# Optimization experiments

Measured on AMD Instinct MI355X. Metric: run time of the kernel, lower is better.

Reference implementation:

```python
import jax, jax.numpy as jnp
import numpy as np

B, R, T = 128, 36, 40
E, V, H1, H2, PH, VOC = 1024, 2048, 1024, 1024, 256, 10000


def _lstm_cell(x, h, c, Wi, Wh, b):
    # torch gate order: i, f, g, o
    g = x @ Wi.T + h @ Wh.T + b
    i, f, gg, o = jnp.split(g, 4, axis=-1)
    c_new = jax.nn.sigmoid(f) * c + jax.nn.sigmoid(i) * jnp.tanh(gg)
    h_new = jax.nn.sigmoid(o) * jnp.tanh(c_new)
    return h_new, c_new


def setup_inputs() -> dict:
    key = jax.random.key(0)
    ks = jax.random.split(key, 20)
    s = 0.05
    Vmat = jax.random.normal(ks[0], (B, R, V), jnp.float32)
    enc_features = jax.random.normal(ks[1], (B, V), jnp.float32)
    union_vfeats = jax.random.normal(ks[2], (B, V), jnp.float32)
    captions = jax.random.randint(ks[3], (B, T), 0, VOC, jnp.int32)
    lengths = jax.random.randint(ks[4], (B,), 1, T + 1, jnp.int32)
    lengths = jnp.sort(lengths)[::-1].at[0].set(T)  # sorted descending, max first
    embed_W = jax.random.normal(ks[5], (VOC, E), jnp.float32) * s
    Wi1 = jax.random.normal(ks[6], (4 * H1, H2 + V + E), jnp.float32) * s
    Wh1 = jax.random.normal(ks[7], (4 * H1, H1), jnp.float32) * s
    b1 = jax.random.normal(ks[8], (4 * H1,), jnp.float32) * s
    Wi2 = jax.random.normal(ks[9], (4 * H2, H1 + V), jnp.float32) * s
    Wh2 = jax.random.normal(ks[10], (4 * H2, H2), jnp.float32) * s
    b2 = jax.random.normal(ks[11], (4 * H2,), jnp.float32) * s
    Wva = jax.random.normal(ks[12], (PH, V), jnp.float32) * s
    bva = jax.random.normal(ks[13], (PH,), jnp.float32) * s
    Wha = jax.random.normal(ks[14], (PH, H1), jnp.float32) * s
    bha = jax.random.normal(ks[15], (PH,), jnp.float32) * s
    wa = jax.random.normal(ks[16], (PH,), jnp.float32) * s
    ba = jax.random.normal(ks[17], (), jnp.float32) * s
    Wl = jax.random.normal(ks[18], (VOC, H2), jnp.float32) * s
    bl = jax.random.normal(ks[19], (VOC,), jnp.float32) * s
    return dict(Vmat=Vmat, enc_features=enc_features, union_vfeats=union_vfeats,
                captions=captions, lengths=lengths, embed_W=embed_W,
                Wi1=Wi1, Wh1=Wh1, b1=b1, Wi2=Wi2, Wh2=Wh2, b2=b2,
                Wva=Wva, bva=bva, Wha=Wha, bha=bha, wa=wa, ba=ba, Wl=Wl, bl=bl)


def reference(Vmat, enc_features, union_vfeats, captions, lengths, embed_W,
              Wi1, Wh1, b1, Wi2, Wh2, b2, Wva, bva, Wha, bha, wa, ba, Wl, bl):
    embeddings = embed_W[captions]                      # [B, T, E]
    Va = Vmat @ Wva.T + bva                             # [B, R, PH] (precompute, step-invariant)

    def step(carry, xs):
        h1, c1, h2, c2 = carry
        emb_t, i = xs
        active = (lengths > i)[:, None]                 # [B, 1]
        x1 = jnp.concatenate([h2, union_vfeats, emb_t], axis=-1)
        h1n, c1n = _lstm_cell(x1, h1, c1, Wi1, Wh1, b1)
        # top-down attention over R regions
        logit = jnp.tanh(Va + (h1n @ Wha.T + bha)[:, None, :]) @ wa + ba  # [B, R]
        atten = jax.nn.softmax(logit, axis=1)
        av = jnp.einsum('br,brd->bd', atten, Vmat)      # [B, V]
        x2 = jnp.concatenate([av, h1n], axis=-1)
        h2n, c2n = _lstm_cell(x2, h2, c2, Wi2, Wh2, b2)
        logits = h2n @ Wl.T + bl                        # [B, VOC]
        # state freeze + zero outputs for finished sequences (ragged masking)
        h1 = jnp.where(active, h1n, h1); c1 = jnp.where(active, c1n, c1)
        h2 = jnp.where(active, h2n, h2); c2 = jnp.where(active, c2n, c2)
        out_t = jnp.where(active, logits, 0.0)
        return (h1, c1, h2, c2), out_t

    z1 = jnp.zeros((B, H1), jnp.float32)
    z2 = jnp.zeros((B, H2), jnp.float32)
    xs = (jnp.transpose(embeddings, (1, 0, 2)), jnp.arange(T, dtype=jnp.int32))
    _, outs = jax.lax.scan(step, (z1, z1, z2, z2), xs)  # [T, B, VOC]
    return jnp.transpose(outs, (1, 0, 2))               # [B, T, VOC]
```

## Files before the change

kernel.cpp:

```cpp
#include <hip/hip_runtime.h>

#define EPI_PART 0
#define EPI_BF16D 1

#define T_ 40
#define VOC_ 10000

typedef __attribute__((ext_vector_type(8))) short bf16x8;
typedef __attribute__((ext_vector_type(4))) short short4v;
typedef __attribute__((ext_vector_type(8))) short short8v;
typedef __attribute__((ext_vector_type(4))) float float4v;
typedef __attribute__((ext_vector_type(4))) float f32x4;

__device__ __forceinline__ float bf2f(short s) {
  unsigned u = ((unsigned)(unsigned short)s) << 16;
  float f; __builtin_memcpy(&f, &u, 4); return f;
}
__device__ __forceinline__ short f2bf(float f) {
  unsigned u; __builtin_memcpy(&u, &f, 4);
  u += 0x7FFFu + ((u >> 16) & 1u);
  return (short)(u >> 16);
}
__device__ __forceinline__ float sigm(float x) { return 1.f / (1.f + expf(-x)); }

__device__ __forceinline__ size_t pkidx(int row, int k, int K) {
  return (size_t)(row >> 4) * 16 * K + (size_t)(k >> 3) * 128 + (size_t)((row & 15) * 8 + (k & 7));
}


__global__ __launch_bounds__(256) void k_f2bf_split(const float* __restrict__ s,
    short* __restrict__ dh, short* __restrict__ dl, long n4) {
  long i = (long)blockIdx.x * 256 + threadIdx.x;
  long stride = (long)gridDim.x * 256;
  for (; i < n4; i += stride) {
    float4v f = ((const float4v*)s)[i];
    short4v oh, ol;
    #pragma unroll
    for (int j = 0; j < 4; j++) {
      short h = f2bf(f[j]); oh[j] = h; ol[j] = f2bf(f[j] - bf2f(h));
    }
    ((short4v*)dh)[i] = oh;
    ((short4v*)dl)[i] = ol;
  }
}

__global__ __launch_bounds__(256) void k_permpk(short* __restrict__ dh, short* __restrict__ dl,
    const float* __restrict__ s1, int ld1, int col0, int K1,
    const float* __restrict__ s2, int ld2, int Ktot) {
  int K4 = Ktot >> 2;
  long n4 = 4096L * K4;
  long stride = (long)gridDim.x * 256;
  for (long i = (long)blockIdx.x * 256 + threadIdx.x; i < n4; i += stride) {
    int p = (int)(i / K4);
    int c = ((int)(i % K4)) << 2;
    int orig = ((p & 3) << 10) + (p >> 2);
    const float* src = (c < K1) ? (s1 + (long)orig * ld1 + col0 + c)
                                : (s2 + (long)orig * ld2 + (c - K1));
    float4v f = *(const float4v*)src;
    short4v oh, ol;
    #pragma unroll
    for (int j = 0; j < 4; j++) {
      short h = f2bf(f[j]); oh[j] = h; ol[j] = f2bf(f[j] - bf2f(h));
    }
    size_t d = pkidx(p, c, Ktot);
    *(short4v*)&dh[d] = oh;
    if (dl) *(short4v*)&dl[d] = ol;
  }
}

__global__ __launch_bounds__(256) void k_packpk(short* __restrict__ dh, short* __restrict__ dl,
    const float* __restrict__ src, int ld, int Nr, int Nsrc, int K) {
  int K4 = K >> 2;
  long n4 = (long)Nr * K4;
  long stride = (long)gridDim.x * 256;
  for (long i = (long)blockIdx.x * 256 + threadIdx.x; i < n4; i += stride) {
    int row = (int)(i / K4);
    int c = ((int)(i % K4)) << 2;
    float4v f = {0.f, 0.f, 0.f, 0.f};
    if (row < Nsrc) f = *(const float4v*)(src + (long)row * ld + c);
    short4v oh, ol;
    #pragma unroll
    for (int j = 0; j < 4; j++) {
      short h = f2bf(f[j]); oh[j] = h; ol[j] = f2bf(f[j] - bf2f(h));
    }
    size_t d = pkidx(row, c, K);
    *(short4v*)&dh[d] = oh;
    if (dl) *(short4v*)&dl[d] = ol;
  }
}

__global__ __launch_bounds__(256) void k_perm_bias(float* __restrict__ d1, const float* __restrict__ s1,
                                                   float* __restrict__ d2, const float* __restrict__ s2) {
  int p = blockIdx.x * 256 + threadIdx.x;
  if (p < 4096) {
    int orig = ((p & 3) << 10) + (p >> 2);
    d1[p] = s1[orig];
    d2[p] = s2[orig];
  }
}

__global__ __launch_bounds__(256) void k_gather_emb(short* __restrict__ dst, const float* __restrict__ embW,
                                                    const int* __restrict__ cap) {
  int i = blockIdx.x * 256 + threadIdx.x;
  if (i >= 5120 * 128) return;
  int row = i >> 7, c8 = (i & 127) << 3;
  int tok = cap[row];
  const float4v* s = (const float4v*)(embW + (long)tok * 1024 + c8);
  float4v f0 = s[0], f1 = s[1];
  short8v o;
  #pragma unroll
  for (int j = 0; j < 4; j++) { o[j] = f2bf(f0[j]); o[4 + j] = f2bf(f1[j]); }
  *(short8v*)(dst + (long)row * 1024 + c8) = o;
}

__global__ __launch_bounds__(256) void k_pack_whaf(float* __restrict__ dst, const float* __restrict__ Wha) {
  int i = blockIdx.x * 256 + threadIdx.x;
  int hb = i >> 8, ph = i & 255;
  float4v a = *(const float4v*)(Wha + (long)ph * 1024 + hb * 8);
  float4v b4 = *(const float4v*)(Wha + (long)ph * 1024 + hb * 8 + 4);
  *(float4v*)(dst + ((long)hb * 256 + ph) * 8) = a;
  *(float4v*)(dst + ((long)hb * 256 + ph) * 8 + 4) = b4;
}


template<int NCS, bool SA, bool SW, int EPI>
__global__ __launch_bounds__(256) void k_g5(
    const short* __restrict__ A, const short* __restrict__ Alo, int lda,
    const short* __restrict__ W, const short* __restrict__ Wlo, int K,
    int Npad, int Mtot,
    float* __restrict__ outf, short* __restrict__ outbf) {
  __shared__ short sh[SA ? 16384 : 8192];
  const int tid = threadIdx.x;
  const int l = tid & 63, w = tid >> 6;
  const int rif = l & 15, kg = l >> 4;
  const int n0 = blockIdx.x * 64;
  const int k0 = blockIdx.y * NCS * 64;
  const int mbase = blockIdx.z * 128;

  f32x4 acc[8];
  #pragma unroll
  for (int m = 0; m < 8; m++) acc[m] = (f32x4){0.f, 0.f, 0.f, 0.f};

  bf16x8 wh[2][2], wl[2][2];
  const size_t wtile = (size_t)(n0 / 16 + w) * 16 * K + (size_t)l * 8;
  auto loadW = [&](int c, int slot) {
    size_t base = wtile + (size_t)((k0 + c * 64) >> 3) * 128;
    #pragma unroll
    for (int sk = 0; sk < 2; sk++) {
      wh[slot][sk] = *(const bf16x8*)(W + base + sk * 512);
      if (SW) wl[slot][sk] = *(const bf16x8*)(Wlo + base + sk * 512);
    }
  };

  short8v rA[4], rL[4];
  const int srow = tid >> 3;
  const int scol = (tid & 7) * 8;
  auto ldA = [&](int c) {
    #pragma unroll
    for (int j = 0; j < 4; j++) {
      size_t g = (size_t)(mbase + j * 32 + srow) * lda + k0 + c * 64 + scol;
      rA[j] = *(const short8v*)(A + g);
      if (SA) rL[j] = *(const short8v*)(Alo + g);
    }
  };
  auto stA = [&]() {
    #pragma unroll
    for (int j = 0; j < 4; j++) {
      int row = j * 32 + srow;
      int idx = row * 64 + (scol ^ ((row & 7) << 3));
      *(short8v*)&sh[idx] = rA[j];
      if (SA) *(short8v*)&sh[8192 + idx] = rL[j];
    }
  };
  auto compute = [&](int slot) {
    #pragma unroll
    for (int sk = 0; sk < 2; sk++) {
      int colb = ((sk * 32 + kg * 8) ^ ((rif & 7) << 3));
      #pragma unroll
      for (int m = 0; m < 8; m++) {
        int idx = (m * 16 + rif) * 64 + colb;
        bf16x8 ah = *(const bf16x8*)&sh[idx];
        acc[m] = __builtin_amdgcn_mfma_f32_16x16x32_bf16(ah, wh[slot][sk], acc[m], 0, 0, 0);
        if (SA) {
          bf16x8 al = *(const bf16x8*)&sh[8192 + idx];
          acc[m] = __builtin_amdgcn_mfma_f32_16x16x32_bf16(al, wh[slot][sk], acc[m], 0, 0, 0);
        }
        if (SW) acc[m] = __builtin_amdgcn_mfma_f32_16x16x32_bf16(ah, wl[slot][sk], acc[m], 0, 0, 0);
      }
    }
  };

  ldA(0); loadW(0, 0);
  stA();
  __syncthreads();
  #pragma unroll
  for (int c = 0; c < NCS; c++) {
    if (c + 1 < NCS) { ldA(c + 1); loadW(c + 1, (c + 1) & 1); }
    compute(c & 1);
    __syncthreads();
    if (c + 1 < NCS) { stA(); __syncthreads(); }
  }

  const int colw = n0 + w * 16 + rif;
  #pragma unroll
  for (int m = 0; m < 8; m++) {
    #pragma unroll
    for (int j = 0; j < 4; j++) {
      int row = m * 16 + kg * 4 + j;
      if constexpr (EPI == EPI_PART) {
        outf[((size_t)blockIdx.y * Mtot + mbase + row) * Npad + colw] = acc[m][j];
      } else {
        outbf[(size_t)(mbase + row) * Npad + colw] = f2bf(acc[m][j]);
      }
    }
  }
}

__global__ __launch_bounds__(256) void k_sum(const float* __restrict__ part,
    float* __restrict__ out, const float* __restrict__ bias,
    long n4, int N4, int KS, long stride4) {
  long i = (long)blockIdx.x * 256 + threadIdx.x;
  if (i >= n4) return;
  float4v a = *(const float4v*)&bias[(i % N4) * 4];
  for (int s = 0; s < KS; s++) {
    float4v p = ((const float4v*)part)[s * stride4 + i];
    #pragma unroll
    for (int j = 0; j < 4; j++) a[j] += p[j];
  }
  ((float4v*)out)[i] = a;
}

__global__ __launch_bounds__(256) void k_epi2(
    const float* __restrict__ part, const float* __restrict__ b2p,
    float* __restrict__ cstate,
    const short* __restrict__ xcur_hi, const short* __restrict__ xcur_lo,
    short* __restrict__ xnext_hi, short* __restrict__ xnext_lo,
    short* __restrict__ h2n_hi, short* __restrict__ h2n_lo,
    const int* __restrict__ lengths, int t) {
  int i = blockIdx.x * 256 + threadIdx.x;
  int b = i >> 10, h = i & 1023;
  float4v g = *(const float4v*)&b2p[h * 4];
  #pragma unroll
  for (int s = 0; s < 8; s++) {
    float4v p = *(const float4v*)&part[((size_t)s * 128 + b) * 4096 + h * 4];
    #pragma unroll
    for (int j = 0; j < 4; j++) g[j] += p[j];
  }
  float co = cstate[b * 1024 + h];
  float cn = sigm(g[1]) * co + sigm(g[0]) * tanhf(g[2]);
  float hn = sigm(g[3]) * tanhf(cn);
  bool act = lengths[b] > t;
  cstate[b * 1024 + h] = act ? cn : co;
  short hi16 = f2bf(hn);
  short lo16 = f2bf(hn - bf2f(hi16));
  h2n_hi[b * 1024 + h] = hi16;
  h2n_lo[b * 1024 + h] = lo16;
  short oh = xcur_hi[b * 2048 + h];
  short ol = xcur_lo[b * 2048 + h];
  xnext_hi[b * 2048 + h] = act ? hi16 : oh;
  xnext_lo[b * 2048 + h] = act ? lo16 : ol;
}

__global__ __launch_bounds__(256) void k_epi_logits(const float* __restrict__ part,
    const float* __restrict__ bl, const int* __restrict__ lengths, int t,
    float* __restrict__ out) {
  int id = blockIdx.x * 256 + threadIdx.x;
  if (id >= 320000) return;
  int b = id / 2500, q = (id % 2500) * 4;
  bool act = lengths[b] > t;
  float4v a = {0.f, 0.f, 0.f, 0.f};
  if (act) {
    a = *(const float4v*)&bl[q];
    #pragma unroll
    for (int s = 0; s < 4; s++) {
      float4v p = *(const float4v*)&part[((size_t)s * 128 + b) * 10048 + q];
      #pragma unroll
      for (int j = 0; j < 4; j++) a[j] += p[j];
    }
  }
  *(float4v*)&out[((size_t)b * T_ + t) * VOC_ + q] = a;
}

__global__ __launch_bounds__(256) void k_attn2(
    const float* __restrict__ partG,
    const float* __restrict__ zuv, const short* __restrict__ zemb,
    float* __restrict__ c1,
    const short* __restrict__ xcH, const short* __restrict__ xcL,
    short* __restrict__ xnH, short* __restrict__ xnL,
    short* __restrict__ x2H, short* __restrict__ x2L,
    const float* __restrict__ WhaF,
    const float* __restrict__ bha, const float* __restrict__ wa,
    const float* __restrict__ ba, const float* __restrict__ Va,
    const float* __restrict__ Vmat,
    const int* __restrict__ lengths, int t) {
  const int b = blockIdx.x, tid = threadIdx.x;
  __shared__ float h1f[1024];
  __shared__ float ha_sh[256];
  __shared__ float wa_sh[256];
  __shared__ float logit_sh[40];
  __shared__ float p_sh[40];
  const bool act = lengths[b] > t;
  #pragma unroll
  for (int i = 0; i < 4; i++) {
    int h = i * 256 + tid;
    float4v g = {0.f, 0.f, 0.f, 0.f};
    #pragma unroll
    for (int s = 0; s < 8; s++) {
      float4v p = *(const float4v*)&partG[((size_t)s * 128 + b) * 4096 + h * 4];
      #pragma unroll
      for (int j = 0; j < 4; j++) g[j] += p[j];
    }
    float4v z = *(const float4v*)&zuv[(size_t)b * 4096 + h * 4];
    short4v e4 = *(const short4v*)&zemb[((size_t)b * T_ + t) * 4096 + h * 4];
    #pragma unroll
    for (int j = 0; j < 4; j++) g[j] += z[j] + bf2f(e4[j]);
    float co = c1[b * 1024 + h];
    float cn = sigm(g[1]) * co + sigm(g[0]) * tanhf(g[2]);
    float hn = sigm(g[3]) * tanhf(cn);
    c1[b * 1024 + h] = act ? cn : co;
    h1f[h] = hn;
    short hi16 = f2bf(hn);
    short lo16 = f2bf(hn - bf2f(hi16));
    x2H[b * 4096 + 2048 + h] = hi16;
    x2L[b * 4096 + 2048 + h] = lo16;
    short oh = xcH[b * 2048 + 1024 + h];
    short ol = xcL[b * 2048 + 1024 + h];
    xnH[b * 2048 + 1024 + h] = act ? hi16 : oh;
    xnL[b * 2048 + 1024 + h] = act ? lo16 : ol;
    x2H[b * 4096 + 3072 + h] = xcH[b * 2048 + h];
    x2L[b * 4096 + 3072 + h] = xcL[b * 2048 + h];
  }
  wa_sh[tid] = wa[tid];
  __syncthreads();
  {
    float a = 0.f;
    const float* wp = WhaF + tid * 8;
    #pragma unroll 4
    for (int hb = 0; hb < 128; hb++) {
      float4v w0 = *(const float4v*)(wp + (size_t)hb * 2048);
      float4v w1 = *(const float4v*)(wp + (size_t)hb * 2048 + 4);
      #pragma unroll
      for (int j = 0; j < 4; j++) a += w0[j] * h1f[hb * 8 + j] + w1[j] * h1f[hb * 8 + 4 + j];
    }
    ha_sh[tid] = a + bha[tid];
  }
  __syncthreads();
  {
    const int r0 = tid >> 3, sl = tid & 7;
    const float ba0 = ba[0];
    for (int r = r0; r < 36; r += 32) {
      const float4v* va4 = (const float4v*)(Va + ((long)b * 36 + r) * 256 + sl * 32);
      float part = 0.f;
      #pragma unroll
      for (int q = 0; q < 8; q++) {
        float4v v4 = va4[q];
        #pragma unroll
        for (int j = 0; j < 4; j++) {
          int ph = sl * 32 + q * 4 + j;
          part += tanhf(v4[j] + ha_sh[ph]) * wa_sh[ph];
        }
      }
      part += __shfl_down(part, 4, 8);
      part += __shfl_down(part, 2, 8);
      part += __shfl_down(part, 1, 8);
      if (sl == 0) logit_sh[r] = part + ba0;
    }
  }
  __syncthreads();
  if (tid < 64) {
    float v = (tid < 36) ? logit_sh[tid] : -3.4e38f;
    float m = v;
    #pragma unroll
    for (int off = 32; off > 0; off >>= 1) m = fmaxf(m, __shfl_xor(m, off));
    float e = (tid < 36) ? expf(v - m) : 0.f;
    float s = e;
    #pragma unroll
    for (int off = 32; off > 0; off >>= 1) s += __shfl_xor(s, off);
    if (tid < 36) p_sh[tid] = e / s;
  }
  __syncthreads();
  {
    float av[8];
    #pragma unroll
    for (int j = 0; j < 8; j++) av[j] = 0.f;
    const float* vb = Vmat + (long)b * (36 * 2048) + tid * 8;
    for (int r = 0; r < 36; r++) {
      float p = p_sh[r];
      float4v v0 = *(const float4v*)(vb + (long)r * 2048);
      float4v v1 = *(const float4v*)(vb + (long)r * 2048 + 4);
      #pragma unroll
      for (int j = 0; j < 4; j++) { av[j] += p * v0[j]; av[4 + j] += p * v1[j]; }
    }
    short8v oh, ol;
    #pragma unroll
    for (int j = 0; j < 8; j++) {
      short h = f2bf(av[j]);
      oh[j] = h;
      ol[j] = f2bf(av[j] - bf2f(h));
    }
    *(short8v*)(x2H + b * 4096 + tid * 8) = oh;
    *(short8v*)(x2L + b * 4096 + tid * 8) = ol;
  }
}

extern "C" void kernel_launch(void* const* d_in, const int* in_sizes, int n_in,
                              void* d_out, int out_size, void* d_ws, size_t ws_size,
                              hipStream_t stream) {
  const float* Vmat = (const float*)d_in[0];
  const float* uv   = (const float*)d_in[2];
  const int* captions = (const int*)d_in[3];
  const int* lengths  = (const int*)d_in[4];
  const float* embW = (const float*)d_in[5];
  const float* Wi1 = (const float*)d_in[6];
  const float* Wh1 = (const float*)d_in[7];
  const float* b1  = (const float*)d_in[8];
  const float* Wi2 = (const float*)d_in[9];
  const float* Wh2 = (const float*)d_in[10];
  const float* b2  = (const float*)d_in[11];
  const float* Wva = (const float*)d_in[12];
  const float* bva = (const float*)d_in[13];
  const float* Wha = (const float*)d_in[14];
  const float* bha = (const float*)d_in[15];
  const float* wa  = (const float*)d_in[16];
  const float* ba  = (const float*)d_in[17];
  const float* Wl  = (const float*)d_in[18];
  const float* bl  = (const float*)d_in[19];
  (void)in_sizes; (void)n_in; (void)out_size; (void)ws_size;

  char* ws = (char*)d_ws;
  size_t off = 0;
  auto alloc = [&](size_t bytes) { void* p = ws + off; off += (bytes + 255) & ~255UL; return p; };
  short* W1dHi = (short*)alloc(4096L * 2048 * 2);
  short* W1dLo = (short*)alloc(4096L * 2048 * 2);
  short* W2dHi = (short*)alloc(4096L * 4096 * 2);
  short* W2dLo = (short*)alloc(4096L * 4096 * 2);
  short* WlPK  = (short*)alloc(10048L * 1024 * 2);
  float* WhaF  = (float*)alloc(128L * 256 * 8 * 4);
  float* VaBuf = (float*)alloc(4608L * 256 * 4);
  float* Z1uvB = (float*)alloc(128L * 4096 * 4);
  short* Z1embB = (short*)alloc(5120L * 4096 * 2);
  float* partG = (float*)alloc(4L * 128 * 10048 * 4);
  float* b1P = (float*)alloc(4096 * 4);
  float* b2P = (float*)alloc(4096 * 4);
  short* x1Hi = (short*)alloc(2L * 128 * 2048 * 2);
  short* x1Lo = (short*)alloc(2L * 128 * 2048 * 2);
  short* x2Hi = (short*)alloc(128L * 4096 * 2);
  short* x2Lo = (short*)alloc(128L * 4096 * 2);
  short* h2nHi = (short*)alloc(128L * 1024 * 2);
  short* h2nLo = (short*)alloc(128L * 1024 * 2);
  float* c1 = (float*)alloc(128L * 1024 * 4);
  float* c2 = (float*)alloc(128L * 1024 * 4);

  short* W1uvHi = W2dHi;
  short* W1uvLo = W2dHi + 4096L * 2048;
  float* zuvPart = (float*)(W2dHi + 4096L * 4096);
  short* uvHi = W2dHi + 4096L * 4096 + 4096L * 2048 + 2097152;
  short* uvLo = uvHi + 128L * 2048;
  short* WvaHi = uvLo + 128L * 2048;
  short* WvaLo = WvaHi + 256L * 2048;
  float* vaPart = (float*)W2dHi;
  short* W1ePk = (short*)partG;
  short* AembBF = (short*)partG + 4096L * 1024;
  short* VmatHi = Z1embB;
  short* VmatLo = Z1embB + 4608L * 2048;

  (void)hipMemsetAsync(x1Hi, 0, 2L * 128 * 2048 * 2, stream);
  (void)hipMemsetAsync(x1Lo, 0, 2L * 128 * 2048 * 2, stream);
  (void)hipMemsetAsync(c1, 0, 128L * 1024 * 4, stream);
  (void)hipMemsetAsync(c2, 0, 128L * 1024 * 4, stream);

  k_packpk<<<2048, 256, 0, stream>>>(WlPK, nullptr, Wl, 1024, 10048, 10000, 1024);
  k_pack_whaf<<<128, 256, 0, stream>>>(WhaF, Wha);
  k_packpk<<<512, 256, 0, stream>>>(WvaHi, WvaLo, Wva, 2048, 256, 256, 2048);
  k_permpk<<<2048, 256, 0, stream>>>(W1dHi, W1dLo, Wi1, 4096, 0, 1024, Wh1, 1024, 2048);
  k_permpk<<<2048, 256, 0, stream>>>(W1uvHi, W1uvLo, Wi1, 4096, 1024, 2048, Wi1, 4096, 2048);
  k_permpk<<<1024, 256, 0, stream>>>(W1ePk, nullptr, Wi1, 4096, 3072, 1024, Wi1, 4096, 1024);
  k_perm_bias<<<16, 256, 0, stream>>>(b1P, b1, b2P, b2);
  k_gather_emb<<<2560, 256, 0, stream>>>(AembBF, embW, captions);
  k_f2bf_split<<<2048, 256, 0, stream>>>(Vmat, VmatHi, VmatLo, 128L * 36 * 2048 / 4);
  k_f2bf_split<<<64, 256, 0, stream>>>(uv, uvHi, uvLo, 128L * 2048 / 4);

  k_g5<4, true, true, EPI_PART><<<dim3(64, 8, 1), 256, 0, stream>>>(
      uvHi, uvLo, 2048, W1uvHi, W1uvLo, 2048, 4096, 128, zuvPart, nullptr);
  k_sum<<<512, 256, 0, stream>>>(zuvPart, Z1uvB, b1P, 131072, 1024, 8, 131072);
  k_g5<4, true, true, EPI_PART><<<dim3(4, 8, 36), 256, 0, stream>>>(
      VmatHi, VmatLo, 2048, WvaHi, WvaLo, 2048, 256, 4608, vaPart, nullptr);
  k_sum<<<1152, 256, 0, stream>>>(vaPart, VaBuf, bva, 294912, 64, 8, 294912);
  k_permpk<<<4096, 256, 0, stream>>>(W2dHi, W2dLo, Wi2, 3072, 0, 3072, Wh2, 1024, 4096);
  k_g5<16, false, false, EPI_BF16D><<<dim3(64, 1, 40), 256, 0, stream>>>(
      AembBF, nullptr, 1024, W1ePk, nullptr, 1024, 4096, 5120, nullptr, Z1embB);

  for (int t = 0; t < T_; t++) {
    const short* xcH = x1Hi + (size_t)(t & 1) * (128 * 2048);
    const short* xcL = x1Lo + (size_t)(t & 1) * (128 * 2048);
    short* xnH = x1Hi + (size_t)((t + 1) & 1) * (128 * 2048);
    short* xnL = x1Lo + (size_t)((t + 1) & 1) * (128 * 2048);
    k_g5<4, true, true, EPI_PART><<<dim3(64, 8, 1), 256, 0, stream>>>(
        xcH, xcL, 2048, W1dHi, W1dLo, 2048, 4096, 128, partG, nullptr);
    k_attn2<<<128, 256, 0, stream>>>(partG, Z1uvB, Z1embB, c1,
        xcH, xcL, xnH, xnL, x2Hi, x2Lo, WhaF, bha, wa, ba, VaBuf, Vmat, lengths, t);
    k_g5<8, true, true, EPI_PART><<<dim3(64, 8, 1), 256, 0, stream>>>(
        x2Hi, x2Lo, 4096, W2dHi, W2dLo, 4096, 4096, 128, partG, nullptr);
    k_epi2<<<512, 256, 0, stream>>>(partG, b2P, c2,
        xcH, xcL, xnH, xnL, h2nHi, h2nLo, lengths, t);
    k_g5<4, true, false, EPI_PART><<<dim3(157, 4, 1), 256, 0, stream>>>(
        h2nHi, h2nLo, 1024, WlPK, nullptr, 1024, 10048, 128, partG, nullptr);
    k_epi_logits<<<1250, 256, 0, stream>>>(partG, bl, lengths, t, (float*)d_out);
  }
}
```

Baseline: 4.154 ms.

## Widen GEMM tiles and overlap vocab projection with next step's LSTM1 GEMM

The GEMM kernel now computes 128-wide N tiles, two 16-column fragments per wave, so each A tile loaded into shared memory is reused across twice as many outputs. The timestep loop is software-pipelined. The output-vocab GEMM for step t-1 runs in the same launch as the LSTM1 gate GEMM for step t, and its epilogue runs alongside the attention kernel, cutting launches and filling the GPU with more concurrent blocks. This needs an extra loop iteration, a padded Wl packing to 10112 columns and separate partial buffers. It also doubles the weight registers per thread, which may lower occupancy.

```diff
diff --git a/kernel.cpp b/kernel.cpp
--- a/kernel.cpp
+++ b/kernel.cpp
@@ -124,31 +124,37 @@
 
 
 template<int NCS, bool SA, bool SW, int EPI>
-__global__ __launch_bounds__(256) void k_g5(
+__device__ __forceinline__ void gemm_body(short* sh, int bx, int ks, int mb,
     const short* __restrict__ A, const short* __restrict__ Alo, int lda,
     const short* __restrict__ W, const short* __restrict__ Wlo, int K,
-    int Npad, int Mtot,
-    float* __restrict__ outf, short* __restrict__ outbf) {
-  __shared__ short sh[SA ? 16384 : 8192];
+    int Npad, int Mtot, float* __restrict__ part, short* __restrict__ outbf) {
   const int tid = threadIdx.x;
   const int l = tid & 63, w = tid >> 6;
   const int rif = l & 15, kg = l >> 4;
-  const int n0 = blockIdx.x * 64;
-  const int k0 = blockIdx.y * NCS * 64;
-  const int mbase = blockIdx.z * 128;
-
-  f32x4 acc[8];
+  const int n0 = bx * 128;
+  const int k0 = ks * NCS * 64;
+  const int mbase = mb * 128;
+
+  f32x4 acc[8][2];
   #pragma unroll
-  for (int m = 0; m < 8; m++) acc[m] = (f32x4){0.f, 0.f, 0.f, 0.f};
-
-  bf16x8 wh[2][2], wl[2][2];
-  const size_t wtile = (size_t)(n0 / 16 + w) * 16 * K + (size_t)l * 8;
+  for (int m = 0; m < 8; m++) {
+    acc[m][0] = (f32x4){0.f, 0.f, 0.f, 0.f};
+    acc[m][1] = (f32x4){0.f, 0.f, 0.f, 0.f};
+  }
+
+  bf16x8 wh[2][2][2], wl[2][2][2];
+  size_t wt0 = (size_t)(n0 / 16 + w * 2) * 16 * K + (size_t)l * 8;
+  size_t wt1 = wt0 + (size_t)16 * K;
   auto loadW = [&](int c, int slot) {
-    size_t base = wtile + (size_t)((k0 + c * 64) >> 3) * 128;
+    size_t base = (size_t)((k0 + c * 64) >> 3) * 128;
     #pragma unroll
     for (int sk = 0; sk < 2; sk++) {
-      wh[slot][sk] = *(const bf16x8*)(W + base + sk * 512);
-      if (SW) wl[slot][sk] = *(const bf16x8*)(Wlo + base + sk * 512);
+      wh[slot][sk][0] = *(const bf16x8*)(W + wt0 + base + sk * 512);
+      wh[slot][sk][1] = *(const bf16x8*)(W + wt1 + base + sk * 512);
+      if (SW) {
+        wl[slot][sk][0] = *(const bf16x8*)(Wlo + wt0 + base + sk * 512);
+        wl[slot][sk][1] = *(const bf16x8*)(Wlo + wt1 + base + sk * 512);
+      }
     }
   };
 
@@ -180,12 +186,14 @@
       for (int m = 0; m < 8; m++) {
         int idx = (m * 16 + rif) * 64 + colb;
         bf16x8 ah = *(const bf16x8*)&sh[idx];
-        acc[m] = __builtin_amdgcn_mfma_f32_16x16x32_bf16(ah, wh[slot][sk], acc[m], 0, 0, 0);
-        if (SA) {
-          bf16x8 al = *(const bf16x8*)&sh[8192 + idx];
-          acc[m] = __builtin_amdgcn_mfma_f32_16x16x32_bf16(al, wh[slot][sk], acc[m], 0, 0, 0);
+        bf16x8 al;
+        if (SA) al = *(const bf16x8*)&sh[8192 + idx];
+        #pragma unroll
+        for (int nf = 0; nf < 2; nf++) {
+          acc[m][nf] = __builtin_amdgcn_mfma_f32_16x16x32_bf16(ah, wh[slot][0][nf] * 0 + wh[slot][sk][nf], acc[m][nf], 0, 0, 0);
+          if (SA) acc[m][nf] = __builtin_amdgcn_mfma_f32_16x16x32_bf16(al, wh[slot][sk][nf], acc[m][nf], 0, 0, 0);
+          if (SW) acc[m][nf] = __builtin_amdgcn_mfma_f32_16x16x32_bf16(ah, wl[slot][sk][nf], acc[m][nf], 0, 0, 0);
         }
-        if (SW) acc[m] = __builtin_amdgcn_mfma_f32_16x16x32_bf16(ah, wl[slot][sk], acc[m], 0, 0, 0);
       }
     }
   };
@@ -201,19 +209,32 @@
     if (c + 1 < NCS) { stA(); __syncthreads(); }
   }
 
-  const int colw = n0 + w * 16 + rif;
   #pragma unroll
-  for (int m = 0; m < 8; m++) {
-    #pragma unroll
-    for (int j = 0; j < 4; j++) {
-      int row = m * 16 + kg * 4 + j;
-      if constexpr (EPI == EPI_PART) {
-        outf[((size_t)blockIdx.y * Mtot + mbase + row) * Npad + colw] = acc[m][j];
-      } else {
-        outbf[(size_t)(mbase + row) * Npad + colw] = f2bf(acc[m][j]);
+  for (int nf = 0; nf < 2; nf++) {
+    int colw = n0 + (w * 2 + nf) * 16 + rif;
+    #pragma unroll
+    for (int m = 0; m < 8; m++) {
+      #pragma unroll
+      for (int j = 0; j < 4; j++) {
+        int row = m * 16 + kg * 4 + j;
+        if constexpr (EPI == EPI_PART) {
+          part[((size_t)ks * Mtot + mbase + row) * Npad + colw] = acc[m][nf][j];
+        } else {
+          outbf[(size_t)(mbase + row) * Npad + colw] = f2bf(acc[m][nf][j]);
+        }
       }
     }
   }
+}
+
+template<int NCS, bool SA, bool SW, int EPI>
+__global__ __launch_bounds__(256) void k_g6(
+    const short* __restrict__ A, const short* __restrict__ Alo, int lda,
+    const short* __restrict__ W, const short* __restrict__ Wlo, int K,
+    int Npad, int Mtot, float* __restrict__ part, short* __restrict__ outbf) {
+  __shared__ short sh[SA ? 16384 : 8192];
+  gemm_body<NCS, SA, SW, EPI>(sh, blockIdx.x, blockIdx.y, blockIdx.z,
+      A, Alo, lda, W, Wlo, K, Npad, Mtot, part, outbf);
 }
 
 __global__ __launch_bounds__(256) void k_sum(const float* __restrict__ part,
@@ -261,44 +282,66 @@
   xnext_lo[b * 2048 + h] = act ? lo16 : ol;
 }
 
-__global__ __launch_bounds__(256) void k_epi_logits(const float* __restrict__ part,
-    const float* __restrict__ bl, const int* __restrict__ lengths, int t,
-    float* __restrict__ out) {
-  int id = blockIdx.x * 256 + threadIdx.x;
-  if (id >= 320000) return;
-  int b = id / 2500, q = (id % 2500) * 4;
-  bool act = lengths[b] > t;
-  float4v a = {0.f, 0.f, 0.f, 0.f};
-  if (act) {
-    a = *(const float4v*)&bl[q];
-    #pragma unroll
-    for (int s = 0; s < 4; s++) {
-      float4v p = *(const float4v*)&part[((size_t)s * 128 + b) * 10048 + q];
-      #pragma unroll
-      for (int j = 0; j < 4; j++) a[j] += p[j];
-    }
-  }
-  *(float4v*)&out[((size_t)b * T_ + t) * VOC_ + q] = a;
-}
-
-__global__ __launch_bounds__(256) void k_attn2(
-    const float* __restrict__ partG,
+__global__ __launch_bounds__(256) void k_dualA(
+    const short* __restrict__ xcH, const short* __restrict__ xcL,
+    const short* __restrict__ W1dHi, const short* __restrict__ W1dLo,
+    float* __restrict__ partA,
+    const short* __restrict__ h2nHi, const short* __restrict__ h2nLo,
+    const short* __restrict__ WlPK, float* __restrict__ partLG, int t) {
+  __shared__ short sh[16384];
+  int bx = blockIdx.x;
+  if (bx < 256) {
+    if (t >= T_) return;
+    gemm_body<4, true, true, EPI_PART>(sh, bx & 31, bx >> 5, 0,
+        xcH, xcL, 2048, W1dHi, W1dLo, 2048, 4096, 128, partA, nullptr);
+  } else {
+    if (t == 0) return;
+    int f = bx - 256;
+    gemm_body<8, true, false, EPI_PART>(sh, f % 79, f / 79, 0,
+        h2nHi, h2nLo, 1024, WlPK, nullptr, 1024, 10112, 128, partLG, nullptr);
+  }
+}
+
+__global__ __launch_bounds__(256) void k_dualB(
+    const float* __restrict__ partA,
     const float* __restrict__ zuv, const short* __restrict__ zemb,
     float* __restrict__ c1,
     const short* __restrict__ xcH, const short* __restrict__ xcL,
     short* __restrict__ xnH, short* __restrict__ xnL,
     short* __restrict__ x2H, short* __restrict__ x2L,
-    const float* __restrict__ WhaF,
-    const float* __restrict__ bha, const float* __restrict__ wa,
-    const float* __restrict__ ba, const float* __restrict__ Va,
-    const float* __restrict__ Vmat,
-    const int* __restrict__ lengths, int t) {
-  const int b = blockIdx.x, tid = threadIdx.x;
+    const float* __restrict__ WhaF, const float* __restrict__ bha,
+    const float* __restrict__ wa, const float* __restrict__ ba,
+    const float* __restrict__ Va, const float* __restrict__ Vmat,
+    const int* __restrict__ lengths,
+    const float* __restrict__ partLG, const float* __restrict__ bl,
+    float* __restrict__ out, int t) {
   __shared__ float h1f[1024];
   __shared__ float ha_sh[256];
   __shared__ float wa_sh[256];
   __shared__ float logit_sh[40];
   __shared__ float p_sh[40];
+  const int tid = threadIdx.x;
+  if (blockIdx.x >= 128) {
+    if (t == 0) return;
+    int id = (blockIdx.x - 128) * 256 + tid;
+    if (id >= 320000) return;
+    int b = id / 2500, q = (id % 2500) * 4;
+    bool act = lengths[b] > (t - 1);
+    float4v a = {0.f, 0.f, 0.f, 0.f};
+    if (act) {
+      a = *(const float4v*)&bl[q];
+      #pragma unroll
+      for (int s = 0; s < 2; s++) {
+        float4v p = *(const float4v*)&partLG[((size_t)s * 128 + b) * 10112 + q];
+        #pragma unroll
+        for (int j = 0; j < 4; j++) a[j] += p[j];
+      }
+    }
+    *(float4v*)&out[((size_t)b * T_ + (t - 1)) * VOC_ + q] = a;
+    return;
+  }
+  if (t >= T_) return;
+  const int b = blockIdx.x;
   const bool act = lengths[b] > t;
   #pragma unroll
   for (int i = 0; i < 4; i++) {
@@ -306,7 +349,7 @@
     float4v g = {0.f, 0.f, 0.f, 0.f};
     #pragma unroll
     for (int s = 0; s < 8; s++) {
-      float4v p = *(const float4v*)&partG[((size_t)s * 128 + b) * 4096 + h * 4];
+      float4v p = *(const float4v*)&partA[((size_t)s * 128 + b) * 4096 + h * 4];
       #pragma unroll
       for (int j = 0; j < 4; j++) g[j] += p[j];
     }
@@ -434,12 +477,13 @@
   short* W1dLo = (short*)alloc(4096L * 2048 * 2);
   short* W2dHi = (short*)alloc(4096L * 4096 * 2);
   short* W2dLo = (short*)alloc(4096L * 4096 * 2);
-  short* WlPK  = (short*)alloc(10048L * 1024 * 2);
+  short* WlPK  = (short*)alloc(10112L * 1024 * 2);
   float* WhaF  = (float*)alloc(128L * 256 * 8 * 4);
   float* VaBuf = (float*)alloc(4608L * 256 * 4);
   float* Z1uvB = (float*)alloc(128L * 4096 * 4);
   short* Z1embB = (short*)alloc(5120L * 4096 * 2);
-  float* partG = (float*)alloc(4L * 128 * 10048 * 4);
+  float* partA = (float*)alloc(8L * 128 * 4096 * 4);
+  float* partLG = (float*)alloc(2L * 128 * 10112 * 4);
   float* b1P = (float*)alloc(4096 * 4);
   float* b2P = (float*)alloc(4096 * 4);
   short* x1Hi = (short*)alloc(2L * 128 * 2048 * 2);
@@ -459,8 +503,8 @@
   short* WvaHi = uvLo + 128L * 2048;
   short* WvaLo = WvaHi + 256L * 2048;
   float* vaPart = (float*)W2dHi;
-  short* W1ePk = (short*)partG;
-  short* AembBF = (short*)partG + 4096L * 1024;
+  short* W1ePk = (short*)partA;
+  short* AembBF = (short*)partA + 4096L * 1024;
   short* VmatHi = Z1embB;
   short* VmatLo = Z1embB + 4608L * 2048;
 
@@ -469,7 +513,7 @@
   (void)hipMemsetAsync(c1, 0, 128L * 1024 * 4, stream);
   (void)hipMemsetAsync(c2, 0, 128L * 1024 * 4, stream);
 
-  k_packpk<<<2048, 256, 0, stream>>>(WlPK, nullptr, Wl, 1024, 10048, 10000, 1024);
+  k_packpk<<<2048, 256, 0, stream>>>(WlPK, nullptr, Wl, 1024, 10112, 10000, 1024);
   k_pack_whaf<<<128, 256, 0, stream>>>(WhaF, Wha);
   k_packpk<<<512, 256, 0, stream>>>(WvaHi, WvaLo, Wva, 2048, 256, 256, 2048);
   k_permpk<<<2048, 256, 0, stream>>>(W1dHi, W1dLo, Wi1, 4096, 0, 1024, Wh1, 1024, 2048);
@@ -480,31 +524,31 @@
   k_f2bf_split<<<2048, 256, 0, stream>>>(Vmat, VmatHi, VmatLo, 128L * 36 * 2048 / 4);
   k_f2bf_split<<<64, 256, 0, stream>>>(uv, uvHi, uvLo, 128L * 2048 / 4);
 
-  k_g5<4, true, true, EPI_PART><<<dim3(64, 8, 1), 256, 0, stream>>>(
+  k_g6<4, true, true, EPI_PART><<<dim3(32, 8, 1), 256, 0, stream>>>(
       uvHi, uvLo, 2048, W1uvHi, W1uvLo, 2048, 4096, 128, zuvPart, nullptr);
   k_sum<<<512, 256, 0, stream>>>(zuvPart, Z1uvB, b1P, 131072, 1024, 8, 131072);
-  k_g5<4, true, true, EPI_PART><<<dim3(4, 8, 36), 256, 0, stream>>>(
+  k_g6<4, true, true, EPI_PART><<<dim3(2, 8, 36), 256, 0, stream>>>(
       VmatHi, VmatLo, 2048, WvaHi, WvaLo, 2048, 256, 4608, vaPart, nullptr);
   k_sum<<<1152, 256, 0, stream>>>(vaPart, VaBuf, bva, 294912, 64, 8, 294912);
   k_permpk<<<4096, 256, 0, stream>>>(W2dHi, W2dLo, Wi2, 3072, 0, 3072, Wh2, 1024, 4096);
-  k_g5<16, false, false, EPI_BF16D><<<dim3(64, 1, 40), 256, 0, stream>>>(
+  k_g6<16, false, false, EPI_BF16D><<<dim3(32, 1, 40), 256, 0, stream>>>(
       AembBF, nullptr, 1024, W1ePk, nullptr, 1024, 4096, 5120, nullptr, Z1embB);
 
-  for (int t = 0; t < T_; t++) {
+  for (int t = 0; t <= T_; t++) {
     const short* xcH = x1Hi + (size_t)(t & 1) * (128 * 2048);
     const short* xcL = x1Lo + (size_t)(t & 1) * (128 * 2048);
     short* xnH = x1Hi + (size_t)((t + 1) & 1) * (128 * 2048);
     short* xnL = x1Lo + (size_t)((t + 1) & 1) * (128 * 2048);
-    k_g5<4, true, true, EPI_PART><<<dim3(64, 8, 1), 256, 0, stream>>>(
-        xcH, xcL, 2048, W1dHi, W1dLo, 2048, 4096, 128, partG, nullptr);
-    k_attn2<<<128, 256, 0, stream>>>(partG, Z1uvB, Z1embB, c1,
-        xcH, xcL, xnH, xnL, x2Hi, x2Lo, WhaF, bha, wa, ba, VaBuf, Vmat, lengths, t);
-    k_g5<8, true, true, EPI_PART><<<dim3(64, 8, 1), 256, 0, stream>>>(
-        x2Hi, x2Lo, 4096, W2dHi, W2dLo, 4096, 4096, 128, partG, nullptr);
-    k_epi2<<<512, 256, 0, stream>>>(partG, b2P, c2,
-        xcH, xcL, xnH, xnL, h2nHi, h2nLo, lengths, t);
-    k_g5<4, true, false, EPI_PART><<<dim3(157, 4, 1), 256, 0, stream>>>(
-        h2nHi, h2nLo, 1024, WlPK, nullptr, 1024, 10048, 128, partG, nullptr);
-    k_epi_logits<<<1250, 256, 0, stream>>>(partG, bl, lengths, t, (float*)d_out);
-  }
-}
+    k_dualA<<<414, 256, 0, stream>>>(xcH, xcL, W1dHi, W1dLo, partA,
+        h2nHi, h2nLo, WlPK, partLG, t);
+    k_dualB<<<1378, 256, 0, stream>>>(partA, Z1uvB, Z1embB, c1,
+        xcH, xcL, xnH, xnL, x2Hi, x2Lo, WhaF, bha, wa, ba, VaBuf, Vmat,
+        lengths, partLG, bl, (float*)d_out, t);
+    if (t < T_) {
+      k_g6<8, true, true, EPI_PART><<<dim3(32, 8, 1), 256, 0, stream>>>(
+          x2Hi, x2Lo, 4096, W2dHi, W2dLo, 4096, 4096, 128, partA, nullptr);
+      k_epi2<<<512, 256, 0, stream>>>(partA, b2P, c2,
+          xcH, xcL, xnH, xnL, h2nHi, h2nLo, lengths, t);
+    }
+  }
+}
```

Result: faster. 3.689 ms (-11.2%).
